# Optimization experiments

Measured on AMD Instinct MI355X. Metric: run time of the kernel, lower is better.

## Reference

```python
import jax, jax.numpy as jnp
import numpy as np


def setup_inputs() -> dict:
    key = jax.random.key(0)
    ks = jax.random.split(key, 8)
    B, C, N = 4, 64, 32768
    d = C // 8
    inp = {
        "x": jax.random.normal(ks[0], (B, C, N), dtype=jnp.float32),
        "Wq": jax.random.normal(ks[1], (d, C), dtype=jnp.float32) * 0.1,
        "bq": jax.random.normal(ks[2], (d,), dtype=jnp.float32) * 0.1,
        "Wk": jax.random.normal(ks[3], (d, C), dtype=jnp.float32) * 0.1,
        "bk": jax.random.normal(ks[4], (d,), dtype=jnp.float32) * 0.1,
        "Wv": jax.random.normal(ks[5], (C, C), dtype=jnp.float32) * 0.1,
        "bv": jax.random.normal(ks[6], (C,), dtype=jnp.float32) * 0.1,
        # nn.Parameter(torch.zeros(1)) in the original; nonzero here so the
        # attention branch actually contributes to the output.
        "gamma": jax.random.normal(ks[7], (1,), dtype=jnp.float32) * 0.1,
        "window_size": 512,
        "stride": 256,
        "pooling_factor": 2,
    }
    return inp


def reference(x, Wq, bq, Wk, bk, Wv, bv, gamma, window_size, stride, pooling_factor):
    B, C, N = x.shape
    # conv1x1 projections are pointwise -> apply once on the full signal
    q = jnp.einsum("dc,bcn->bdn", Wq, x) + bq[None, :, None]  # [B, d, N]
    k = jnp.einsum("dc,bcn->bdn", Wk, x) + bk[None, :, None]  # [B, d, N]
    v = jnp.einsum("ec,bcn->ben", Wv, x) + bv[None, :, None]  # [B, C, N]

    starts = jnp.arange(0, N - window_size + 1, stride)              # [W]
    idx = starts[:, None] + jnp.arange(window_size)[None, :]         # [W, ws]

    qw = q[:, :, idx]  # [B, d, W, ws]
    kw = k[:, :, idx]
    vw = v[:, :, idx]  # [B, C, W, ws]
    xw = x[:, :, idx]

    energy = jnp.einsum("bdwi,bdwj->bwij", qw, kw)                   # [B, W, ws, ws]
    attn = jax.nn.softmax(energy, axis=-1)
    # torch: bmm(v, attn^T) -> out[c,i] = sum_j v[c,j] * attn[i,j]
    out_local = jnp.einsum("bcwj,bwij->bcwi", vw, attn)              # [B, C, W, ws]

    contrib = gamma[0] * out_local + xw
    out = jnp.zeros_like(x).at[:, :, idx].add(contrib)               # overlap-add
    counts = jnp.zeros((N,), x.dtype).at[idx].add(1.0)               # overlap count
    out = out / counts[None, None, :]

    P = pooling_factor
    Np = (N // P) * P
    out = out[:, :, :Np].reshape(B, C, N // P, P).max(axis=-1)       # MaxPool1d(P)
    return out
```

## Files before the change

### kernel.cpp

```cpp
#include <hip/hip_runtime.h>
#include <hip/hip_bf16.h>

#define BB 4
#define CC 64
#define DD 8
#define NN 32768
#define WW 512
#define STR 256
#define NWIN 127
#define LOG2E 1.4426950408889634f

typedef short bf16x8 __attribute__((ext_vector_type(8)));
typedef float f32x4 __attribute__((ext_vector_type(4)));
typedef float f32x16 __attribute__((ext_vector_type(16)));

__device__ __forceinline__ unsigned int pack_bf16(float lo, float hi) {
    __hip_bfloat162 h = __float22bfloat162_rn(make_float2(lo, hi));
    unsigned int r; __builtin_memcpy(&r, &h, 4);
    return r;
}
__device__ __forceinline__ unsigned short to_bf16(float f) {
    __hip_bfloat16 h = __float2bfloat16(f);
    unsigned short r; __builtin_memcpy(&r, &h, 2);
    return r;
}
__device__ __forceinline__ float bf2f(unsigned short s) {
    union { unsigned int u; float f; } v; v.u = ((unsigned int)s) << 16;
    return v.f;
}
__device__ __forceinline__ float fast_exp2(float x) {
#if __has_builtin(__builtin_amdgcn_exp2f)
    return __builtin_amdgcn_exp2f(x);
#else
    float r; asm("v_exp_f32 %0, %1" : "=v"(r) : "v"(x)); return r;
#endif
}
__device__ __forceinline__ void plswap(unsigned int &x, unsigned int &y) {
    asm("v_permlane32_swap_b32 %0, %1" : "+v"(x), "+v"(y));
}
__device__ __forceinline__ bf16x8 pack8(float a0, float a1, float a2, float a3,
                                        float a4, float a5, float a6, float a7) {
    union { bf16x8 v; unsigned int u[4]; } r;
    r.u[0] = pack_bf16(a0, a1); r.u[1] = pack_bf16(a2, a3);
    r.u[2] = pack_bf16(a4, a5); r.u[3] = pack_bf16(a6, a7);
    return r.v;
}
__device__ __forceinline__ bf16x8 words4(unsigned int w0, unsigned int w1,
                                         unsigned int w2, unsigned int w3) {
    union { bf16x8 v; unsigned int u[4]; } r;
    r.u[0] = w0; r.u[1] = w1; r.u[2] = w2; r.u[3] = w3;
    return r.v;
}

__global__ __launch_bounds__(256) void qkv_kernel(
    const float* __restrict__ x,
    const float* __restrict__ Wq, const float* __restrict__ bq,
    const float* __restrict__ Wk, const float* __restrict__ bk,
    const float* __restrict__ Wv, const float* __restrict__ bv,
    unsigned short* __restrict__ qout, unsigned short* __restrict__ kout,
    unsigned short* __restrict__ vout)
{
    const int t = threadIdx.x;
    const int lane = t & 63, wv = t >> 6;
    const int a = lane & 15, g = lane >> 4;

    bf16x8 wf[5][2];
    #pragma unroll
    for (int T = 0; T < 5; ++T) {
        const float* wrow;
        float scale = 1.f;
        if (T == 0) {
            if (a < 8) { wrow = Wq + a*CC; scale = LOG2E; }
            else       { wrow = Wk + (a-8)*CC; }
        } else {
            wrow = Wv + ((T-1)*16 + a)*CC;
        }
        #pragma unroll
        for (int h = 0; h < 2; ++h) {
            float4 w0 = *(const float4*)(wrow + h*32 + g*8);
            float4 w1 = *(const float4*)(wrow + h*32 + g*8 + 4);
            wf[T][h] = pack8(w0.x*scale, w0.y*scale, w0.z*scale, w0.w*scale,
                             w1.x*scale, w1.y*scale, w1.z*scale, w1.w*scale);
        }
    }
    f32x4 bias[5];
    {
        const int r = g*4;
        #pragma unroll
        for (int u = 0; u < 4; ++u) {
            int rr = r + u;
            bias[0][u] = (rr < 8) ? bq[rr]*LOG2E : bk[rr-8];
        }
        #pragma unroll
        for (int T = 1; T < 5; ++T)
            #pragma unroll
            for (int u = 0; u < 4; ++u)
                bias[T][u] = bv[(T-1)*16 + r + u];
    }

    const int wave_id = blockIdx.x*4 + wv;
    #pragma unroll 1
    for (int it = 0; it < 2; ++it) {
        const int chunk = wave_id + it*4096;
        const int b = chunk >> 11;
        const int n0 = (chunk & 2047) * 16;
        const int n = n0 + a;
        const float* xcol = x + (size_t)b*CC*NN + n;

        float xv0[8], xv1[8];
        #pragma unroll
        for (int u = 0; u < 8; ++u) xv0[u] = xcol[(size_t)(g*8 + u)*NN];
        #pragma unroll
        for (int u = 0; u < 8; ++u) xv1[u] = xcol[(size_t)(32 + g*8 + u)*NN];
        bf16x8 xb0 = pack8(xv0[0],xv0[1],xv0[2],xv0[3],xv0[4],xv0[5],xv0[6],xv0[7]);
        bf16x8 xb1 = pack8(xv1[0],xv1[1],xv1[2],xv1[3],xv1[4],xv1[5],xv1[6],xv1[7]);

        f32x4 acc[5];
        #pragma unroll
        for (int T = 0; T < 5; ++T) {
            acc[T] = __builtin_amdgcn_mfma_f32_16x16x32_bf16(wf[T][0], xb0, bias[T], 0, 0, 0);
            acc[T] = __builtin_amdgcn_mfma_f32_16x16x32_bf16(wf[T][1], xb1, acc[T], 0, 0, 0);
        }

        {
            unsigned int lo = pack_bf16(acc[0][0], acc[0][1]);
            unsigned int hi = pack_bf16(acc[0][2], acc[0][3]);
            unsigned short* base = ((g < 2) ? qout : kout) + ((size_t)b*NN + n)*8 + (g & 1)*4;
            *(int2*)base = make_int2((int)lo, (int)hi);
        }
        #pragma unroll
        for (int T = 1; T < 5; ++T) {
            #pragma unroll
            for (int u = 0; u < 4; ++u) {
                const int e = (T-1)*16 + g*4 + u;
                vout[((size_t)b*CC + e)*NN + n] = to_bf16(acc[T][u]);
            }
        }
    }
}

__global__ __launch_bounds__(256) void attn_kernel(
    const unsigned short* __restrict__ qg, const unsigned short* __restrict__ kg,
    const unsigned short* __restrict__ vg,
    unsigned short* __restrict__ accE, unsigned short* __restrict__ accO)
{
    __shared__ float sInv[4][2][32];
    const int t = threadIdx.x;
    const int lane = t & 63, wv = t >> 6;
    const int l31 = lane & 31, hi = lane >> 5;
    int bid = (blockIdx.x & 7)*127 + (blockIdx.x >> 3);
    const int ih = bid & 1; bid >>= 1;
    const int w = bid % NWIN, b = bid / NWIN;
    const int nwin = STR * w;
    const int i0 = ih*256 + wv*64;

    const unsigned short* qbase = qg + ((size_t)b*NN + nwin + i0)*8;
    const unsigned short* kbase = kg + ((size_t)b*NN + nwin)*8;
    const unsigned short* vbase = vg + (size_t)b*CC*NN + nwin;

    const bf16x8 zf = {};
    bf16x8 qf[2];
    #pragma unroll
    for (int it = 0; it < 2; ++it) {
        bf16x8 raw = *(const bf16x8*)(qbase + (size_t)(it*32 + l31)*8);
        qf[it] = hi ? zf : raw;
    }
    bf16x8 kc = *(const bf16x8*)(kbase + (size_t)l31*8);

    f32x16 acc[2][2] = {};
    float2 rsum2[2] = {make_float2(0.f,0.f), make_float2(0.f,0.f)};

    for (int jt = 0; jt < 16; ++jt) {
        const int j0 = jt*32;
        bf16x8 vf[2][2];
        #pragma unroll
        for (int ct = 0; ct < 2; ++ct)
            #pragma unroll
            for (int sl = 0; sl < 2; ++sl)
                vf[ct][sl] = *(const bf16x8*)(vbase + (size_t)(ct*32 + l31)*NN + j0 + sl*16 + hi*8);
        bf16x8 kn = kc;
        if (jt < 15) kn = *(const bf16x8*)(kbase + (size_t)(j0 + 32 + l31)*8);

        #pragma unroll
        for (int it = 0; it < 2; ++it) {
            __builtin_amdgcn_s_setprio(1);
            const f32x16 z16 = {};
            f32x16 E = __builtin_amdgcn_mfma_f32_32x32x16_bf16(kc, qf[it], z16, 0, 0, 0);
            float p[16];
            #pragma unroll
            for (int r = 0; r < 16; ++r) p[r] = fast_exp2(E[r]);
            float2 s0 = make_float2(p[0],  p[1])  + make_float2(p[2],  p[3]);
            float2 s1 = make_float2(p[4],  p[5])  + make_float2(p[6],  p[7]);
            float2 s2 = make_float2(p[8],  p[9])  + make_float2(p[10], p[11]);
            float2 s3 = make_float2(p[12], p[13]) + make_float2(p[14], p[15]);
            rsum2[it] += (s0 + s1) + (s2 + s3);
            unsigned int wd[8];
            #pragma unroll
            for (int tw = 0; tw < 8; ++tw) wd[tw] = pack_bf16(p[2*tw], p[2*tw+1]);
            unsigned int F0 = wd[0], F2 = wd[2]; plswap(F0, F2);
            unsigned int F1 = wd[1], F3 = wd[3]; plswap(F1, F3);
            unsigned int G0 = wd[4], G2 = wd[6]; plswap(G0, G2);
            unsigned int G1 = wd[5], G3 = wd[7]; plswap(G1, G3);
            bf16x8 pa0 = words4(F0, F1, F2, F3);
            bf16x8 pa1 = words4(G0, G1, G2, G3);
            #pragma unroll
            for (int ct = 0; ct < 2; ++ct) {
                acc[it][ct] = __builtin_amdgcn_mfma_f32_32x32x16_bf16(pa0, vf[ct][0], acc[it][ct], 0, 0, 0);
                acc[it][ct] = __builtin_amdgcn_mfma_f32_32x32x16_bf16(pa1, vf[ct][1], acc[it][ct], 0, 0, 0);
            }
            __builtin_amdgcn_s_setprio(0);
        }
        kc = kn;
    }

    float rsum[2];
    #pragma unroll
    for (int it = 0; it < 2; ++it) {
        float r = rsum2[it].x + rsum2[it].y;
        r += __shfl_xor(r, 32);
        rsum[it] = r;
    }
    if (lane < 32) {
        sInv[wv][0][lane] = 1.f / rsum[0];
        sInv[wv][1][lane] = 1.f / rsum[1];
    }
    f32x4 invv[2][4];
    #pragma unroll
    for (int it = 0; it < 2; ++it)
        #pragma unroll
        for (int g = 0; g < 4; ++g)
            invv[it][g] = *(const f32x4*)&sInv[wv][it][8*g + 4*hi];

    unsigned short* ob = ((w & 1) ? accO : accE) + (size_t)b*CC*NN + nwin + i0;
    #pragma unroll
    for (int it = 0; it < 2; ++it) {
        #pragma unroll
        for (int ct = 0; ct < 2; ++ct) {
            unsigned short* cbase = ob + (size_t)(ct*32 + l31)*NN + it*32;
            #pragma unroll
            for (int g = 0; g < 4; ++g) {
                float a0 = acc[it][ct][4*g+0] * invv[it][g][0];
                float a1 = acc[it][ct][4*g+1] * invv[it][g][1];
                float a2 = acc[it][ct][4*g+2] * invv[it][g][2];
                float a3 = acc[it][ct][4*g+3] * invv[it][g][3];
                int2 pw = make_int2((int)pack_bf16(a0, a1), (int)pack_bf16(a2, a3));
                *(int2*)(cbase + 8*g + 4*hi) = pw;
            }
        }
    }
}

__global__ __launch_bounds__(256) void final_kernel(
    const float* __restrict__ x,
    const unsigned short* __restrict__ accE, const unsigned short* __restrict__ accO,
    const float* __restrict__ gamma, float* __restrict__ out)
{
    const size_t tid = (size_t)blockIdx.x*256 + threadIdx.x;
    const size_t base = tid*8;
    const int n = (int)(base & (NN-1));
    const float g = gamma[0];

    float xv[8];
    *(float4*)&xv[0] = *(const float4*)&x[base];
    *(float4*)&xv[4] = *(const float4*)&x[base+4];
    int4 aeq = *(const int4*)&accE[base];
    const unsigned int* ae = (const unsigned int*)&aeq;

    float s[8];
    if (n >= STR && n < NN - STR) {
        int4 aoq = *(const int4*)&accO[base];
        const unsigned int* ao = (const unsigned int*)&aoq;
        #pragma unroll
        for (int u = 0; u < 4; ++u) {
            float e0 = bf2f((unsigned short)(ae[u] & 0xffff));
            float e1 = bf2f((unsigned short)(ae[u] >> 16));
            float o0 = bf2f((unsigned short)(ao[u] & 0xffff));
            float o1 = bf2f((unsigned short)(ao[u] >> 16));
            s[2*u]   = fmaf(g, (e0 + o0)*0.5f, xv[2*u]);
            s[2*u+1] = fmaf(g, (e1 + o1)*0.5f, xv[2*u+1]);
        }
    } else {
        #pragma unroll
        for (int u = 0; u < 4; ++u) {
            float e0 = bf2f((unsigned short)(ae[u] & 0xffff));
            float e1 = bf2f((unsigned short)(ae[u] >> 16));
            s[2*u]   = fmaf(g, e0, xv[2*u]);
            s[2*u+1] = fmaf(g, e1, xv[2*u+1]);
        }
    }
    float4 o = make_float4(fmaxf(s[0], s[1]), fmaxf(s[2], s[3]),
                           fmaxf(s[4], s[5]), fmaxf(s[6], s[7]));
    *(float4*)&out[tid*4] = o;
}

extern "C" void kernel_launch(void* const* d_in, const int* in_sizes, int n_in,
                              void* d_out, int out_size, void* d_ws, size_t ws_size,
                              hipStream_t stream)
{
    const float* x    = (const float*)d_in[0];
    const float* Wq   = (const float*)d_in[1];
    const float* bq   = (const float*)d_in[2];
    const float* Wk   = (const float*)d_in[3];
    const float* bk   = (const float*)d_in[4];
    const float* Wv   = (const float*)d_in[5];
    const float* bv   = (const float*)d_in[6];
    const float* gamma= (const float*)d_in[7];

    unsigned short* q    = (unsigned short*)d_ws;
    unsigned short* k    = q + (size_t)BB*NN*DD;
    unsigned short* v    = k + (size_t)BB*NN*DD;
    unsigned short* accE = v + (size_t)BB*CC*NN;
    unsigned short* accO = accE + (size_t)BB*CC*NN;
    float* out = (float*)d_out;

    qkv_kernel<<<1024, 256, 0, stream>>>(x, Wq, bq, Wk, bk, Wv, bv, q, k, v);
    attn_kernel<<<BB*NWIN*2, 256, 0, stream>>>(q, k, v, accE, accO);
    final_kernel<<<BB*CC*NN/8/256, 256, 0, stream>>>(x, accE, accO, gamma, out);
}
```

Baseline: 79.86 us.

## Stage K and V tiles through double-buffered LDS shared by all waves

The attention kernel now loads the whole K window into shared memory once, and streams V tiles through a double-buffered LDS array with a register prefetch. Previously each of the four waves read K and V straight from global memory. This removes redundant global loads of V across waves and replaces strided global reads with LDS reads. In exchange it adds a __syncthreads per tile iteration, LDS bank pressure from the padded 36-element rows, and it drops the s_setprio hints.

```diff
diff --git a/kernel.cpp b/kernel.cpp
--- a/kernel.cpp
+++ b/kernel.cpp
@@ -144,6 +144,8 @@
     const unsigned short* __restrict__ vg,
     unsigned short* __restrict__ accE, unsigned short* __restrict__ accO)
 {
+    __shared__ unsigned short sK[WW][8];
+    __shared__ unsigned short sV[2][64][36];
     __shared__ float sInv[4][2][32];
     const int t = threadIdx.x;
     const int lane = t & 63, wv = t >> 6;
@@ -156,7 +158,19 @@
 
     const unsigned short* qbase = qg + ((size_t)b*NN + nwin + i0)*8;
     const unsigned short* kbase = kg + ((size_t)b*NN + nwin)*8;
-    const unsigned short* vbase = vg + (size_t)b*CC*NN + nwin;
+    const unsigned short* vsrc  = vg + ((size_t)b*CC + (t >> 2))*NN + nwin + (t & 3)*8;
+
+    #pragma unroll
+    for (int m = 0; m < 2; ++m) {
+        const int row = m*256 + t;
+        *(int4*)&sK[row][0] = *(const int4*)(kbase + (size_t)row*8);
+    }
+    {
+        int4 r = *(const int4*)vsrc;
+        unsigned short* dst = &sV[0][t >> 2][(t & 3)*8];
+        *(int2*)dst = *(int2*)&r;
+        *(int2*)(dst + 4) = *((int2*)&r + 1);
+    }
 
     const bf16x8 zf = {};
     bf16x8 qf[2];
@@ -165,25 +179,33 @@
         bf16x8 raw = *(const bf16x8*)(qbase + (size_t)(it*32 + l31)*8);
         qf[it] = hi ? zf : raw;
     }
-    bf16x8 kc = *(const bf16x8*)(kbase + (size_t)l31*8);
 
     f32x16 acc[2][2] = {};
     float2 rsum2[2] = {make_float2(0.f,0.f), make_float2(0.f,0.f)};
 
+    __syncthreads();
+
     for (int jt = 0; jt < 16; ++jt) {
         const int j0 = jt*32;
+        const int cur = jt & 1;
+        int4 stg;
+        if (jt < 15) stg = *(const int4*)(vsrc + j0 + 32);
+
+        bf16x8 kc = *(const bf16x8*)&sK[j0 + l31][0];
         bf16x8 vf[2][2];
         #pragma unroll
         for (int ct = 0; ct < 2; ++ct)
             #pragma unroll
-            for (int sl = 0; sl < 2; ++sl)
-                vf[ct][sl] = *(const bf16x8*)(vbase + (size_t)(ct*32 + l31)*NN + j0 + sl*16 + hi*8);
-        bf16x8 kn = kc;
-        if (jt < 15) kn = *(const bf16x8*)(kbase + (size_t)(j0 + 32 + l31)*8);
+            for (int sl = 0; sl < 2; ++sl) {
+                const unsigned short* p = &sV[cur][ct*32 + l31][sl*16 + hi*8];
+                union { bf16x8 v; int2 d[2]; } u;
+                u.d[0] = *(const int2*)p;
+                u.d[1] = *(const int2*)(p + 4);
+                vf[ct][sl] = u.v;
+            }
 
         #pragma unroll
         for (int it = 0; it < 2; ++it) {
-            __builtin_amdgcn_s_setprio(1);
             const f32x16 z16 = {};
             f32x16 E = __builtin_amdgcn_mfma_f32_32x32x16_bf16(kc, qf[it], z16, 0, 0, 0);
             float p[16];
@@ -208,9 +230,14 @@
                 acc[it][ct] = __builtin_amdgcn_mfma_f32_32x32x16_bf16(pa0, vf[ct][0], acc[it][ct], 0, 0, 0);
                 acc[it][ct] = __builtin_amdgcn_mfma_f32_32x32x16_bf16(pa1, vf[ct][1], acc[it][ct], 0, 0, 0);
             }
-            __builtin_amdgcn_s_setprio(0);
-        }
-        kc = kn;
+        }
+
+        if (jt < 15) {
+            unsigned short* dst = &sV[cur ^ 1][t >> 2][(t & 3)*8];
+            *(int2*)dst = *(int2*)&stg;
+            *(int2*)(dst + 4) = *((int2*)&stg + 1);
+        }
+        __syncthreads();
     }
 
     float rsum[2];
```

New measurement: 78.64 us. No clear change (-1.5%).
